# Performance work log

Hardware: AMD Instinct MI355X
Metric: run time of the kernel (lower is better)

The kernel has to match this reference:

```python
import jax, jax.numpy as jnp
import numpy as np

B, G, H = 16, 1708, 5


def setup_inputs() -> dict:
    key = jax.random.key(0)
    k0, k1, k2, k3 = jax.random.split(key, 4)
    x = jax.random.normal(k0, (B, G), dtype=jnp.float32)
    # xavier_normal on (H, G, 1): std = gain*sqrt(2/(fan_in+fan_out)) ~ gain*sqrt(2/G)
    std_qk = 5.0 * np.sqrt(2.0 / (G + 1))   # gain=5 for WQ, WK
    std_v = 1.0 * np.sqrt(2.0 / (G + 1))    # gain=1 for WV
    WQ = jax.random.normal(k1, (H, G, 1), dtype=jnp.float32) * std_qk
    WK = jax.random.normal(k2, (H, G, 1), dtype=jnp.float32) * std_qk
    WV = jax.random.normal(k3, (H, G, 1), dtype=jnp.float32) * std_v
    W0 = jnp.ones((H,), dtype=jnp.float32)  # torch.Tensor(n_head*[1])
    return {"x": x, "WQ": WQ, "WK": WK, "WV": WV, "W0": W0}


def reference(x, WQ, WK, WV, W0):
    # x: (B, G); WQ/WK/WV: (H, G, 1); W0: (H,)
    g = x.shape[1]
    off_diag = 1.0 - jnp.eye(g, dtype=x.dtype)  # mask applied AFTER softmax
    head_outs = []
    for h in range(WQ.shape[0]):  # small fixed head loop keeps peak memory low
        q = x * WQ[h, :, 0]  # (B, G)
        k = x * WK[h, :, 0]  # (B, G)
        v = x * WV[h, :, 0]  # (B, G)
        # scores[b,i,j] = q[b,i] * k[b,j]  (broadcast outer product, not dot-product)
        scores = q[:, :, None] * k[:, None, :]  # (B, G, G)
        z = jax.nn.softmax(scores, axis=2) * off_diag
        head_outs.append(jnp.einsum('bij,bj->bi', z, v))  # (B, G)
    out_seq = jnp.stack(head_outs, axis=-1)  # (B, G, H)
    return jnp.einsum('bgh,h->bg', out_seq, W0)  # (B, G)
```

## Files before the change

kernel.cpp:

```cpp
#include <hip/hip_runtime.h>

constexpr int B = 16;
constexpr int G = 1708;
constexpr int H = 5;
constexpr int M1 = 13;
constexpr int JS = 4;
constexpr int JPS = G / JS;
constexpr int TPB1 = 256;
constexpr int TPB2 = 256;

#define LOG2E 1.4426950408889634f


__device__ __forceinline__ float fast_exp(float x) {
#if __has_builtin(__builtin_amdgcn_exp2f)
    return __builtin_amdgcn_exp2f(x * LOG2E);
#else
    return __expf(x);
#endif
}

__device__ __forceinline__ float fast_rcp(float x) {
#if __has_builtin(__builtin_amdgcn_rcpf)
    return __builtin_amdgcn_rcpf(x);
#else
    return 1.0f / x;
#endif
}

__constant__ float INVFACT[M1] = {
    (float)(1.0),                    (float)(1.0),
    (float)(1.0 / 2.0),              (float)(1.0 / 6.0),
    (float)(1.0 / 24.0),             (float)(1.0 / 120.0),
    (float)(1.0 / 720.0),            (float)(1.0 / 5040.0),
    (float)(1.0 / 40320.0),          (float)(1.0 / 362880.0),
    (float)(1.0 / 3628800.0),        (float)(1.0 / 39916800.0),
    (float)(1.0 / 479001600.0)
};

__global__ __launch_bounds__(TPB1)
void moments_kernel(const float* __restrict__ x,
                    const float* __restrict__ WK,
                    const float* __restrict__ WV,
                    float* __restrict__ g_mom)
{
    const int slice = blockIdx.x % JS;
    const int h     = (blockIdx.x / JS) % H;
    const int b     = blockIdx.x / (JS * H);
    const int j0    = slice * JPS;

    const float* __restrict__ xb = x  + b * G;
    const float* __restrict__ wk = WK + h * G;
    const float* __restrict__ wv = WV + h * G;

    float S[M1], T[M1];
#pragma unroll
    for (int m = 0; m < M1; ++m) { S[m] = 0.f; T[m] = 0.f; }

    for (int t = threadIdx.x; t < JPS; t += TPB1) {
        const int j   = j0 + t;
        const float xj = xb[j];
        const float k  = xj * wk[j];
        const float v  = xj * wv[j];
        const float k2 = k * k;
        const float k4 = k2 * k2;
        float p0 = 1.f, p1 = k, p2 = k2, p3 = k2 * k;
#pragma unroll
        for (int gblk = 0; gblk < 3; ++gblk) {
            const int base = gblk * 4;
            S[base + 0] += p0; T[base + 0] = fmaf(v, p0, T[base + 0]); p0 *= k4;
            S[base + 1] += p1; T[base + 1] = fmaf(v, p1, T[base + 1]); p1 *= k4;
            S[base + 2] += p2; T[base + 2] = fmaf(v, p2, T[base + 2]); p2 *= k4;
            S[base + 3] += p3; T[base + 3] = fmaf(v, p3, T[base + 3]); p3 *= k4;
        }
        S[12] += p0; T[12] = fmaf(v, p0, T[12]);
    }

#pragma unroll
    for (int m = 0; m < M1; ++m) {
#pragma unroll
        for (int off = 8; off <= 32; off <<= 1) {
            S[m] += __shfl_xor(S[m], off, 64);
            T[m] += __shfl_xor(T[m], off, 64);
        }
    }

    __shared__ float red[4 * 8][2 * M1];
    const int wave = threadIdx.x >> 6;
    const int lane = threadIdx.x & 63;
    if (lane < 8) {
        const int row = wave * 8 + lane;
#pragma unroll
        for (int m = 0; m < M1; ++m) {
            red[row][m]      = S[m];
            red[row][M1 + m] = T[m];
        }
    }
    __syncthreads();

    if (threadIdx.x < 2 * M1) {
        const int m = threadIdx.x % M1;
        float s0 = 0.f, s1 = 0.f, s2 = 0.f, s3 = 0.f;
#pragma unroll
        for (int r = 0; r < 32; r += 4) {
            s0 += red[r + 0][threadIdx.x];
            s1 += red[r + 1][threadIdx.x];
            s2 += red[r + 2][threadIdx.x];
            s3 += red[r + 3][threadIdx.x];
        }
        const float s = ((s0 + s1) + (s2 + s3)) * INVFACT[m];
        g_mom[((b * H + h) * (2 * M1) + threadIdx.x) * JS + slice] = s;
    }
}

__global__ __launch_bounds__(TPB2)
void eval_kernel(const float* __restrict__ x,
                 const float* __restrict__ WQ,
                 const float* __restrict__ WK,
                 const float* __restrict__ WV,
                 const float* __restrict__ W0,
                 const float* __restrict__ g_mom,
                 float* __restrict__ out)
{
    __shared__ __align__(16) float mom[H * 32];

    const int b = blockIdx.y;
    const int i = blockIdx.x * TPB2 + threadIdx.x;

    const float4* __restrict__ gm4 =
        (const float4*)g_mom + b * (H * 2 * M1);

    for (int c = threadIdx.x; c < H * 32; c += TPB2) {
        const int h = c >> 5;
        const int s = c & 31;
        float val = 0.f;
        if (s < M1 || (s >= 16 && s < 16 + M1)) {
            const int cc = (s < 16) ? s : (s - 3);
            const float4 p = gm4[h * (2 * M1) + cc];
            val = (p.x + p.y) + (p.z + p.w);
        }
        mom[c] = val;
    }
    __syncthreads();

    if (i >= G) return;

    const float xi = x[b * G + i];
    float acc = 0.f;

#pragma unroll
    for (int h = 0; h < H; ++h) {
        const float q = xi * WQ[h * G + i];

        float Dm[16], Nm[16];
#pragma unroll
        for (int r = 0; r < 4; ++r) {
            *(float4*)&Dm[4 * r] = *(const float4*)&mom[h * 32 + 4 * r];
            *(float4*)&Nm[4 * r] = *(const float4*)&mom[h * 32 + 16 + 4 * r];
        }

        float D = Dm[M1 - 1];
        float N = Nm[M1 - 1];
#pragma unroll
        for (int m = M1 - 2; m >= 0; --m) {
            D = fmaf(D, q, Dm[m]);
            N = fmaf(N, q, Nm[m]);
        }

        const float k   = xi * WK[h * G + i];
        const float v   = xi * WV[h * G + i];
        const float eii = fast_exp(q * k);
        acc = fmaf(W0[h], (N - eii * v) * fast_rcp(D), acc);
    }
    out[b * G + i] = acc;
}

extern "C" void kernel_launch(void* const* d_in, const int* in_sizes, int n_in,
                              void* d_out, int out_size, void* d_ws, size_t ws_size,
                              hipStream_t stream) {
    const float* x  = (const float*)d_in[0];
    const float* WQ = (const float*)d_in[1];
    const float* WK = (const float*)d_in[2];
    const float* WV = (const float*)d_in[3];
    const float* W0 = (const float*)d_in[4];
    float* out   = (float*)d_out;
    float* g_mom = (float*)d_ws;

    moments_kernel<<<B * H * JS, TPB1, 0, stream>>>(x, WK, WV, g_mom);

    dim3 grid2((G + TPB2 - 1) / TPB2, B);
    eval_kernel<<<grid2, TPB2, 0, stream>>>(x, WQ, WK, WV, W0, g_mom, out);
}
```

Before: 66.30 us.

## Fuse moments and eval kernels into one launch with flag-based inter-block sync

New measurement: 70.54 us. 1.06x slower.

```diff
diff --git a/kernel.cpp b/kernel.cpp
--- a/kernel.cpp
+++ b/kernel.cpp
@@ -6,8 +6,11 @@
 constexpr int M1 = 13;
 constexpr int JS = 4;
 constexpr int JPS = G / JS;
-constexpr int TPB1 = 256;
-constexpr int TPB2 = 256;
+constexpr int TPB = 256;
+constexpr int NMOM  = B * H * JS;
+constexpr int EVB   = (G + TPB - 1) / TPB;
+constexpr int NEVAL = B * EVB;
+#define SENT 0x1ACEB00Cu
 
 #define LOG2E 1.4426950408889634f
 
@@ -38,141 +41,167 @@
     (float)(1.0 / 479001600.0)
 };
 
-__global__ __launch_bounds__(TPB1)
-void moments_kernel(const float* __restrict__ x,
-                    const float* __restrict__ WK,
-                    const float* __restrict__ WV,
-                    float* __restrict__ g_mom)
+__global__ __launch_bounds__(TPB, 2)
+void fused_kernel(const float* __restrict__ x,
+                  const float* __restrict__ WQ,
+                  const float* __restrict__ WK,
+                  const float* __restrict__ WV,
+                  const float* __restrict__ W0,
+                  float* __restrict__ g_mom,
+                  unsigned* __restrict__ flags,
+                  float* __restrict__ out)
 {
-    const int slice = blockIdx.x % JS;
-    const int h     = (blockIdx.x / JS) % H;
-    const int b     = blockIdx.x / (JS * H);
-    const int j0    = slice * JPS;
-
-    const float* __restrict__ xb = x  + b * G;
-    const float* __restrict__ wk = WK + h * G;
-    const float* __restrict__ wv = WV + h * G;
-
-    float S[M1], T[M1];
-#pragma unroll
-    for (int m = 0; m < M1; ++m) { S[m] = 0.f; T[m] = 0.f; }
-
-    for (int t = threadIdx.x; t < JPS; t += TPB1) {
-        const int j   = j0 + t;
-        const float xj = xb[j];
-        const float k  = xj * wk[j];
-        const float v  = xj * wv[j];
-        const float k2 = k * k;
-        const float k4 = k2 * k2;
-        float p0 = 1.f, p1 = k, p2 = k2, p3 = k2 * k;
-#pragma unroll
-        for (int gblk = 0; gblk < 3; ++gblk) {
-            const int base = gblk * 4;
-            S[base + 0] += p0; T[base + 0] = fmaf(v, p0, T[base + 0]); p0 *= k4;
-            S[base + 1] += p1; T[base + 1] = fmaf(v, p1, T[base + 1]); p1 *= k4;
-            S[base + 2] += p2; T[base + 2] = fmaf(v, p2, T[base + 2]); p2 *= k4;
-            S[base + 3] += p3; T[base + 3] = fmaf(v, p3, T[base + 3]); p3 *= k4;
-        }
-        S[12] += p0; T[12] = fmaf(v, p0, T[12]);
+    __shared__ float red[4 * 8][2 * M1];
+    __shared__ __align__(16) float mom[H * 32];
+
+    const int tid = threadIdx.x;
+
+    if (blockIdx.x < NMOM) {
+        const int mblk  = blockIdx.x;
+        const int slice = mblk % JS;
+        const int h     = (mblk / JS) % H;
+        const int b     = mblk / (JS * H);
+        const int j0    = slice * JPS;
+
+        const float* __restrict__ xb = x  + b * G;
+        const float* __restrict__ wk = WK + h * G;
+        const float* __restrict__ wv = WV + h * G;
+
+        float S[M1], T[M1];
+#pragma unroll
+        for (int m = 0; m < M1; ++m) { S[m] = 0.f; T[m] = 0.f; }
+
+        for (int t = tid; t < JPS; t += TPB) {
+            const int j    = j0 + t;
+            const float xj = xb[j];
+            const float k  = xj * wk[j];
+            const float v  = xj * wv[j];
+            const float k2 = k * k;
+            const float k4 = k2 * k2;
+            float p0 = 1.f, p1 = k, p2 = k2, p3 = k2 * k;
+#pragma unroll
+            for (int gblk = 0; gblk < 3; ++gblk) {
+                const int base = gblk * 4;
+                S[base + 0] += p0; T[base + 0] = fmaf(v, p0, T[base + 0]); p0 *= k4;
+                S[base + 1] += p1; T[base + 1] = fmaf(v, p1, T[base + 1]); p1 *= k4;
+                S[base + 2] += p2; T[base + 2] = fmaf(v, p2, T[base + 2]); p2 *= k4;
+                S[base + 3] += p3; T[base + 3] = fmaf(v, p3, T[base + 3]); p3 *= k4;
+            }
+            S[12] += p0; T[12] = fmaf(v, p0, T[12]);
+        }
+
+#pragma unroll
+        for (int m = 0; m < M1; ++m) {
+#pragma unroll
+            for (int off = 8; off <= 32; off <<= 1) {
+                S[m] += __shfl_xor(S[m], off, 64);
+                T[m] += __shfl_xor(T[m], off, 64);
+            }
+        }
+
+        const int wave = tid >> 6;
+        const int lane = tid & 63;
+        if (lane < 8) {
+            const int row = wave * 8 + lane;
+#pragma unroll
+            for (int m = 0; m < M1; ++m) {
+                red[row][m]      = S[m];
+                red[row][M1 + m] = T[m];
+            }
+        }
+        __syncthreads();
+
+        if (tid < 2 * M1) {
+            const int m = tid % M1;
+            float s0 = 0.f, s1 = 0.f, s2 = 0.f, s3 = 0.f;
+#pragma unroll
+            for (int r = 0; r < 32; r += 4) {
+                s0 += red[r + 0][tid];
+                s1 += red[r + 1][tid];
+                s2 += red[r + 2][tid];
+                s3 += red[r + 3][tid];
+            }
+            const float s = ((s0 + s1) + (s2 + s3)) * INVFACT[m];
+            g_mom[((b * H + h) * (2 * M1) + tid) * JS + slice] = s;
+        }
+        if (tid == 0) {
+            __hip_atomic_store(&flags[mblk], SENT, __ATOMIC_RELEASE,
+                               __HIP_MEMORY_SCOPE_AGENT);
+        }
+    } else {
+        const int e   = blockIdx.x - NMOM;
+        const int b   = e / EVB;
+        const int blk = e % EVB;
+        const int i   = blk * TPB + tid;
+        const bool act = i < G;
+
+        float xi = 0.f, wq[H], wk[H], wv[H];
+        if (act) {
+            xi = x[b * G + i];
+#pragma unroll
+            for (int h = 0; h < H; ++h) {
+                wq[h] = WQ[h * G + i];
+                wk[h] = WK[h * G + i];
+                wv[h] = WV[h * G + i];
+            }
+        }
+        float w0r[H];
+#pragma unroll
+        for (int h = 0; h < H; ++h) w0r[h] = W0[h];
+
+        if (tid < H * JS) {
+            const unsigned* f = &flags[b * (H * JS) + tid];
+            while (__hip_atomic_load(f, __ATOMIC_ACQUIRE,
+                                     __HIP_MEMORY_SCOPE_AGENT) != SENT) {
+                __builtin_amdgcn_s_sleep(2);
+            }
+        }
+        __syncthreads();
+
+        const float4* __restrict__ gm4 =
+            (const float4*)g_mom + b * (H * 2 * M1);
+        for (int c = tid; c < H * 32; c += TPB) {
+            const int h = c >> 5;
+            const int s = c & 31;
+            float val = 0.f;
+            if (s < M1 || (s >= 16 && s < 16 + M1)) {
+                const int cc = (s < 16) ? s : (s - 3);
+                const float4 p = gm4[h * (2 * M1) + cc];
+                val = (p.x + p.y) + (p.z + p.w);
+            }
+            mom[c] = val;
+        }
+        __syncthreads();
+
+        if (!act) return;
+
+        float acc = 0.f;
+#pragma unroll
+        for (int h = 0; h < H; ++h) {
+            const float q = xi * wq[h];
+
+            float Dm[16], Nm[16];
+#pragma unroll
+            for (int r = 0; r < 4; ++r) {
+                *(float4*)&Dm[4 * r] = *(const float4*)&mom[h * 32 + 4 * r];
+                *(float4*)&Nm[4 * r] = *(const float4*)&mom[h * 32 + 16 + 4 * r];
+            }
+
+            float D = Dm[M1 - 1];
+            float N = Nm[M1 - 1];
+#pragma unroll
+            for (int m = M1 - 2; m >= 0; --m) {
+                D = fmaf(D, q, Dm[m]);
+                N = fmaf(N, q, Nm[m]);
+            }
+
+            const float k   = xi * wk[h];
+            const float v   = xi * wv[h];
+            const float eii = fast_exp(q * k);
+            acc = fmaf(w0r[h], (N - eii * v) * fast_rcp(D), acc);
+        }
+        out[b * G + i] = acc;
     }
-
-#pragma unroll
-    for (int m = 0; m < M1; ++m) {
-#pragma unroll
-        for (int off = 8; off <= 32; off <<= 1) {
-            S[m] += __shfl_xor(S[m], off, 64);
-            T[m] += __shfl_xor(T[m], off, 64);
-        }
-    }
-
-    __shared__ float red[4 * 8][2 * M1];
-    const int wave = threadIdx.x >> 6;
-    const int lane = threadIdx.x & 63;
-    if (lane < 8) {
-        const int row = wave * 8 + lane;
-#pragma unroll
-        for (int m = 0; m < M1; ++m) {
-            red[row][m]      = S[m];
-            red[row][M1 + m] = T[m];
-        }
-    }
-    __syncthreads();
-
-    if (threadIdx.x < 2 * M1) {
-        const int m = threadIdx.x % M1;
-        float s0 = 0.f, s1 = 0.f, s2 = 0.f, s3 = 0.f;
-#pragma unroll
-        for (int r = 0; r < 32; r += 4) {
-            s0 += red[r + 0][threadIdx.x];
-            s1 += red[r + 1][threadIdx.x];
-            s2 += red[r + 2][threadIdx.x];
-            s3 += red[r + 3][threadIdx.x];
-        }
-        const float s = ((s0 + s1) + (s2 + s3)) * INVFACT[m];
-        g_mom[((b * H + h) * (2 * M1) + threadIdx.x) * JS + slice] = s;
-    }
-}
-
-__global__ __launch_bounds__(TPB2)
-void eval_kernel(const float* __restrict__ x,
-                 const float* __restrict__ WQ,
-                 const float* __restrict__ WK,
-                 const float* __restrict__ WV,
-                 const float* __restrict__ W0,
-                 const float* __restrict__ g_mom,
-                 float* __restrict__ out)
-{
-    __shared__ __align__(16) float mom[H * 32];
-
-    const int b = blockIdx.y;
-    const int i = blockIdx.x * TPB2 + threadIdx.x;
-
-    const float4* __restrict__ gm4 =
-        (const float4*)g_mom + b * (H * 2 * M1);
-
-    for (int c = threadIdx.x; c < H * 32; c += TPB2) {
-        const int h = c >> 5;
-        const int s = c & 31;
-        float val = 0.f;
-        if (s < M1 || (s >= 16 && s < 16 + M1)) {
-            const int cc = (s < 16) ? s : (s - 3);
-            const float4 p = gm4[h * (2 * M1) + cc];
-            val = (p.x + p.y) + (p.z + p.w);
-        }
-        mom[c] = val;
-    }
-    __syncthreads();
-
-    if (i >= G) return;
-
-    const float xi = x[b * G + i];
-    float acc = 0.f;
-
-#pragma unroll
-    for (int h = 0; h < H; ++h) {
-        const float q = xi * WQ[h * G + i];
-
-        float Dm[16], Nm[16];
-#pragma unroll
-        for (int r = 0; r < 4; ++r) {
-            *(float4*)&Dm[4 * r] = *(const float4*)&mom[h * 32 + 4 * r];
-            *(float4*)&Nm[4 * r] = *(const float4*)&mom[h * 32 + 16 + 4 * r];
-        }
-
-        float D = Dm[M1 - 1];
-        float N = Nm[M1 - 1];
-#pragma unroll
-        for (int m = M1 - 2; m >= 0; --m) {
-            D = fmaf(D, q, Dm[m]);
-            N = fmaf(N, q, Nm[m]);
-        }
-
-        const float k   = xi * WK[h * G + i];
-        const float v   = xi * WV[h * G + i];
-        const float eii = fast_exp(q * k);
-        acc = fmaf(W0[h], (N - eii * v) * fast_rcp(D), acc);
-    }
-    out[b * G + i] = acc;
 }
 
 extern "C" void kernel_launch(void* const* d_in, const int* in_sizes, int n_in,
@@ -185,9 +214,8 @@
     const float* W0 = (const float*)d_in[4];
     float* out   = (float*)d_out;
     float* g_mom = (float*)d_ws;
-
-    moments_kernel<<<B * H * JS, TPB1, 0, stream>>>(x, WK, WV, g_mom);
-
-    dim3 grid2((G + TPB2 - 1) / TPB2, B);
-    eval_kernel<<<grid2, TPB2, 0, stream>>>(x, WQ, WK, WV, W0, g_mom, out);
-}
+    unsigned* flags = (unsigned*)(g_mom + B * H * 2 * M1 * JS);
+
+    fused_kernel<<<NMOM + NEVAL, TPB, 0, stream>>>(x, WQ, WK, WV, W0,
+                                                   g_mom, flags, out);
+}
```
